# Performance work log

Hardware: AMD Instinct MI355X
Metric: run time of the kernel (lower is better)

The kernel has to match this reference:

```python
import jax, jax.numpy as jnp
import numpy as np

N_NODES = 100000
N_EDGES = 1600000
F_IN, F_HID, F_OUT = 128, 128, 40


def setup_inputs() -> dict:
    key = jax.random.key(0)
    ks = jax.random.split(key, 8)
    x = jax.random.normal(ks[0], (N_NODES, F_IN), dtype=jnp.float32)
    edge_index = jax.random.randint(ks[1], (2, N_EDGES), 0, N_NODES, dtype=jnp.int64)
    # GCNConv weights (glorot-style scale); biases zero per bias_init=zeros_
    W0 = jax.random.normal(ks[2], (F_IN, F_HID), dtype=jnp.float32) / np.sqrt(F_IN)
    b0 = jnp.zeros((F_HID,), dtype=jnp.float32)
    W1 = jax.random.normal(ks[3], (F_HID, F_HID), dtype=jnp.float32) / np.sqrt(F_HID)
    b1 = jnp.zeros((F_HID,), dtype=jnp.float32)
    W2 = jax.random.normal(ks[4], (F_HID, F_OUT), dtype=jnp.float32) / np.sqrt(F_HID)
    b2 = jnp.zeros((F_OUT,), dtype=jnp.float32)
    return {"x": x, "edge_index": edge_index, "W0": W0, "b0": b0,
            "W1": W1, "b1": b1, "W2": W2, "b2": b2}


def _gcn_conv(h, src, dst, W, b):
    # PyG GCNConv (normalize=False, add_self_loops=False):
    # linear transform, then sum-aggregate source features at destinations.
    h = h @ W                                   # [N, F_out]
    msgs = jnp.take(h, src, axis=0)             # [E, F_out] gather
    agg = jax.ops.segment_sum(msgs, dst, num_segments=N_NODES)  # scatter-add
    return agg + b


def reference(x, edge_index, W0, b0, W1, b1, W2, b2):
    src, dst = edge_index[0], edge_index[1]     # flow: source -> target
    h = jax.nn.relu(_gcn_conv(x, src, dst, W0, b0))
    h = jax.nn.relu(_gcn_conv(h, src, dst, W1, b1))
    out = _gcn_conv(h, src, dst, W2, b2)        # last layer: no activation
    return out
```

## Files before the change

### kernel.cpp

```cpp
#include <hip/hip_runtime.h>


typedef short bf16x8 __attribute__((ext_vector_type(8)));
typedef float f32x4  __attribute__((ext_vector_type(4)));

#define EPB 4096

__device__ __forceinline__ float bflo(unsigned int v) {
  union { float f; unsigned int i; } w; w.i = v << 16; return w.f;
}
__device__ __forceinline__ float bfhi(unsigned int v) {
  union { float f; unsigned int i; } w; w.i = v & 0xffff0000u; return w.f;
}
__device__ __forceinline__ unsigned short f2bf(float f) {
  union { float f; unsigned int i; } w; w.f = f;
  unsigned int b = w.i;
  unsigned int r = (b + 0x7fffu + ((b >> 16) & 1u)) >> 16;
  return (unsigned short)r;
}

__device__ __forceinline__ int edge_at(const void* ei, int is64, long long pos) {
  if (is64) return (int)((const long long*)ei)[pos];
  return ((const int*)ei)[pos];
}

__global__ void k_detect(const int* __restrict__ ei32, int* __restrict__ flag) {
  int tid = threadIdx.x;
  int v = ei32[2 * tid + 1];
  unsigned long long m = __ballot(v != 0);
  if (tid == 0) flag[0] = (m == 0ull) ? 1 : 0;
}

__global__ void k_cvt(const float* __restrict__ in, unsigned short* __restrict__ out,
                      long long n4) {
  long long i = (long long)blockIdx.x * blockDim.x + threadIdx.x;
  if (i >= n4) return;
  float4 v = *reinterpret_cast<const float4*>(in + i * 4);
  ushort4 o;
  o.x = f2bf(v.x); o.y = f2bf(v.y); o.z = f2bf(v.z); o.w = f2bf(v.w);
  *reinterpret_cast<ushort4*>(out + i * 4) = o;
}

__global__ void k_wt(const float* __restrict__ W, unsigned short* __restrict__ Wt,
                     int F, int Fp) {
  int idx = blockIdx.x * blockDim.x + threadIdx.x;
  if (idx >= Fp * 128) return;
  int c = idx >> 7, k = idx & 127;
  Wt[c * 128 + k] = (c < F) ? f2bf(W[(size_t)k * F + c]) : (unsigned short)0;
}

__global__ __launch_bounds__(256) void b_hist(const void* __restrict__ ei,
                                              const int* __restrict__ flag, int E,
                                              int* __restrict__ bhist,
                                              int NBKT, int NBLKE) {
  __shared__ int h[512];
  int blk = blockIdx.x, tid = threadIdx.x;
  for (int i = tid; i < NBKT; i += 256) h[i] = 0;
  __syncthreads();
  int is64 = flag[0];
  int base = blk * EPB;
  int cnt = min(EPB, E - base);
  for (int i = tid; i < cnt; i += 256) {
    int d = edge_at(ei, is64, (long long)E + base + i);
    atomicAdd(&h[d >> 8], 1);
  }
  __syncthreads();
  for (int i = tid; i < NBKT; i += 256) bhist[i * NBLKE + blk] = h[i];
}

__global__ void k_scan_a(const int* __restrict__ vals, int* __restrict__ lscan,
                         int* __restrict__ partials, int n) {
  __shared__ int sm[256];
  int tid = threadIdx.x;
  int i = blockIdx.x * 256 + tid;
  int v = (i < n) ? vals[i] : 0;
  sm[tid] = v;
  __syncthreads();
  for (int off = 1; off < 256; off <<= 1) {
    int t = (tid >= off) ? sm[tid - off] : 0;
    __syncthreads();
    sm[tid] += t;
    __syncthreads();
  }
  if (i < n) lscan[i] = sm[tid];
  if (tid == 255) partials[blockIdx.x] = sm[255];
}

__global__ void k_scan_b(int* __restrict__ partials, int nb) {
  __shared__ int sm[1024];
  int tid = threadIdx.x;
  int v = (tid < nb) ? partials[tid] : 0;
  sm[tid] = v;
  __syncthreads();
  for (int off = 1; off < 1024; off <<= 1) {
    int t = (tid >= off) ? sm[tid - off] : 0;
    __syncthreads();
    sm[tid] += t;
    __syncthreads();
  }
  if (tid < nb) partials[tid] = sm[tid] - v;
}

__global__ void k_scan_c(const int* __restrict__ lscan, const int* __restrict__ vals,
                         const int* __restrict__ partials, int* __restrict__ scanned,
                         int n) {
  int i = blockIdx.x * 256 + threadIdx.x;
  if (i >= n) return;
  scanned[i] = lscan[i] - vals[i] + partials[blockIdx.x];
}

__global__ void b_bptr(const int* __restrict__ scanned, int* __restrict__ bucketPtr,
                       int NBKT, int NBLKE, int E) {
  int i = blockIdx.x * 256 + threadIdx.x;
  if (i < NBKT) bucketPtr[i] = scanned[i * NBLKE];
  if (i == 0) bucketPtr[NBKT] = E;
}

__global__ __launch_bounds__(256) void b_scatter(const void* __restrict__ ei,
                                                 const int* __restrict__ flag, int E,
                                                 const int* __restrict__ scanned,
                                                 uint2* __restrict__ ebuf,
                                                 int NBKT, int NBLKE) {
  __shared__ int base[512];
  int blk = blockIdx.x, tid = threadIdx.x;
  for (int i = tid; i < NBKT; i += 256) base[i] = scanned[i * NBLKE + blk];
  __syncthreads();
  int is64 = flag[0];
  int b0 = blk * EPB;
  int cnt = min(EPB, E - b0);
  for (int i = tid; i < cnt; i += 256) {
    int d = edge_at(ei, is64, (long long)E + b0 + i);
    int s = edge_at(ei, is64, b0 + i);
    int pos = atomicAdd(&base[d >> 8], 1);
    ebuf[pos] = make_uint2((unsigned)d, (unsigned)s);
  }
}

__global__ __launch_bounds__(256) void b_pass2(const uint2* __restrict__ ebuf,
                                               const int* __restrict__ bucketPtr,
                                               int* __restrict__ rowptr,
                                               int* __restrict__ colsrc,
                                               int N, int NBKT, int E) {
  __shared__ int hist[256], excl[256], cur[256], sm[256];
  int b = blockIdx.x, tid = threadIdx.x;
  hist[tid] = 0;
  __syncthreads();
  int beg = bucketPtr[b], end = bucketPtr[b + 1];
  for (int i = beg + tid; i < end; i += 256)
    atomicAdd(&hist[ebuf[i].x & 255], 1);
  __syncthreads();
  int v = hist[tid];
  sm[tid] = v;
  __syncthreads();
  for (int off = 1; off < 256; off <<= 1) {
    int t = (tid >= off) ? sm[tid - off] : 0;
    __syncthreads();
    sm[tid] += t;
    __syncthreads();
  }
  excl[tid] = sm[tid] - v;
  cur[tid] = 0;
  __syncthreads();
  int nb0 = b << 8;
  if (nb0 + tid < N) rowptr[nb0 + tid] = beg + excl[tid];
  if (b == 0 && tid == 0) rowptr[N] = E;
  for (int i = beg + tid; i < end; i += 256) {
    uint2 e2 = ebuf[i];
    int dl = (int)(e2.x & 255u);
    int r = atomicAdd(&cur[dl], 1);
    colsrc[beg + excl[dl] + r] = (int)e2.y;
  }
}

__global__ void k_agg128b(const unsigned int* __restrict__ H,
                          const int* __restrict__ rowptr, const int* __restrict__ colsrc,
                          unsigned int* __restrict__ out, int N) {
  int node = blockIdx.x * 4 + (threadIdx.x >> 6);
  if (node >= N) return;
  int l = threadIdx.x & 63;
  int sub = l >> 4, fl = l & 15;
  int beg = rowptr[node], end = rowptr[node + 1];
  float a[8] = {0.f, 0.f, 0.f, 0.f, 0.f, 0.f, 0.f, 0.f};
  int i = beg + sub;
  for (; i + 4 < end; i += 8) {
    int s0 = colsrc[i], s1 = colsrc[i + 4];
    uint4 v0 = *reinterpret_cast<const uint4*>(H + (size_t)s0 * 64 + fl * 4);
    uint4 v1 = *reinterpret_cast<const uint4*>(H + (size_t)s1 * 64 + fl * 4);
    a[0] += bflo(v0.x) + bflo(v1.x); a[1] += bfhi(v0.x) + bfhi(v1.x);
    a[2] += bflo(v0.y) + bflo(v1.y); a[3] += bfhi(v0.y) + bfhi(v1.y);
    a[4] += bflo(v0.z) + bflo(v1.z); a[5] += bfhi(v0.z) + bfhi(v1.z);
    a[6] += bflo(v0.w) + bflo(v1.w); a[7] += bfhi(v0.w) + bfhi(v1.w);
  }
  if (i < end) {
    uint4 v = *reinterpret_cast<const uint4*>(H + (size_t)colsrc[i] * 64 + fl * 4);
    a[0] += bflo(v.x); a[1] += bfhi(v.x);
    a[2] += bflo(v.y); a[3] += bfhi(v.y);
    a[4] += bflo(v.z); a[5] += bfhi(v.z);
    a[6] += bflo(v.w); a[7] += bfhi(v.w);
  }
  #pragma unroll
  for (int k = 0; k < 8; ++k) {
    a[k] += __shfl_xor(a[k], 16);
    a[k] += __shfl_xor(a[k], 32);
  }
  if (sub == 0) {
    uint4 o;
    o.x = ((unsigned)f2bf(a[1]) << 16) | f2bf(a[0]);
    o.y = ((unsigned)f2bf(a[3]) << 16) | f2bf(a[2]);
    o.z = ((unsigned)f2bf(a[5]) << 16) | f2bf(a[4]);
    o.w = ((unsigned)f2bf(a[7]) << 16) | f2bf(a[6]);
    *reinterpret_cast<uint4*>(out + (size_t)node * 64 + fl * 4) = o;
  }
}

__global__ void k_agg40(const unsigned int* __restrict__ T,
                        const int* __restrict__ rowptr, const int* __restrict__ colsrc,
                        const float* __restrict__ b2, float* __restrict__ out, int N) {
  int node = blockIdx.x * 4 + (threadIdx.x >> 6);
  if (node >= N) return;
  int l = threadIdx.x & 63;
  int sub = l >> 4, fl = l & 15;
  int beg = rowptr[node], end = rowptr[node + 1];
  float a[4] = {0.f, 0.f, 0.f, 0.f};
  if (fl < 12) {
    int i = beg + sub;
    for (; i + 4 < end; i += 8) {
      int s0 = colsrc[i], s1 = colsrc[i + 4];
      uint2 v0 = *reinterpret_cast<const uint2*>(T + (size_t)s0 * 24 + fl * 2);
      uint2 v1 = *reinterpret_cast<const uint2*>(T + (size_t)s1 * 24 + fl * 2);
      a[0] += bflo(v0.x) + bflo(v1.x); a[1] += bfhi(v0.x) + bfhi(v1.x);
      a[2] += bflo(v0.y) + bflo(v1.y); a[3] += bfhi(v0.y) + bfhi(v1.y);
    }
    if (i < end) {
      uint2 v = *reinterpret_cast<const uint2*>(T + (size_t)colsrc[i] * 24 + fl * 2);
      a[0] += bflo(v.x); a[1] += bfhi(v.x);
      a[2] += bflo(v.y); a[3] += bfhi(v.y);
    }
  }
  #pragma unroll
  for (int k = 0; k < 4; ++k) {
    a[k] += __shfl_xor(a[k], 16);
    a[k] += __shfl_xor(a[k], 32);
  }
  if (sub == 0 && fl < 10) {
    float4 o;
    o.x = a[0] + b2[fl * 4 + 0];
    o.y = a[1] + b2[fl * 4 + 1];
    o.z = a[2] + b2[fl * 4 + 2];
    o.w = a[3] + b2[fl * 4 + 3];
    *reinterpret_cast<float4*>(out + (size_t)node * 40 + fl * 4) = o;
  }
}

__global__ __launch_bounds__(256) void k_gemm(const unsigned short* __restrict__ A,
                                              const unsigned short* __restrict__ Wt,
                                              const float* __restrict__ bias,
                                              unsigned short* __restrict__ C,
                                              int N, int Fp, int relu) {
  int tid = threadIdx.x;
  int w = tid >> 6, l = tid & 63;
  int r0 = blockIdx.x * 64 + w * 16;
  int arow = r0 + (l & 15);
  if (arow >= N) arow = N - 1;
  int kk = (l >> 4) * 8;
  bf16x8 a[4];
  #pragma unroll
  for (int ks = 0; ks < 4; ++ks)
    a[ks] = *reinterpret_cast<const bf16x8*>(A + (size_t)arow * 128 + ks * 32 + kk);

  int crow0 = r0 + (l >> 4) * 4;
  int ccol = l & 15;
  for (int cf = 0; cf < Fp / 16; ++cf) {
    f32x4 acc = {0.f, 0.f, 0.f, 0.f};
    const unsigned short* wp = Wt + (size_t)(cf * 16 + ccol) * 128 + kk;
    #pragma unroll
    for (int ks = 0; ks < 4; ++ks) {
      bf16x8 b = *reinterpret_cast<const bf16x8*>(wp + ks * 32);
      acc = __builtin_amdgcn_mfma_f32_16x16x32_bf16(a[ks], b, acc, 0, 0, 0);
    }
    float bv = bias ? bias[cf * 16 + ccol] : 0.f;
    #pragma unroll
    for (int r = 0; r < 4; ++r) {
      int gr = crow0 + r;
      if (gr >= N) continue;
      float v = acc[r] + bv;
      if (relu) v = fmaxf(v, 0.f);
      C[(size_t)gr * Fp + cf * 16 + ccol] = f2bf(v);
    }
  }
}

extern "C" void kernel_launch(void* const* d_in, const int* in_sizes, int n_in,
                              void* d_out, int out_size, void* d_ws, size_t ws_size,
                              hipStream_t stream) {
  const float* x  = (const float*)d_in[0];
  const void*  ei = d_in[1];
  const float* W0 = (const float*)d_in[2];
  const float* b0 = (const float*)d_in[3];
  const float* W1 = (const float*)d_in[4];
  const float* b1 = (const float*)d_in[5];
  const float* W2 = (const float*)d_in[6];
  const float* b2 = (const float*)d_in[7];
  float* out = (float*)d_out;

  const int N = in_sizes[0] / 128;
  const int E = in_sizes[1] / 2;
  const int FOUT = in_sizes[6] / 128;
  const int FP3 = 48;

  const int NBLKE = (E + EPB - 1) / EPB;
  const int NBKT  = (N + 255) / 256;
  const int T     = NBKT * NBLKE;
  const int GS    = (T + 255) / 256;

  char* wp = (char*)d_ws;
  auto alloc = [&](size_t bytes) -> void* {
    void* p = (void*)wp;
    wp += (bytes + 255) & ~(size_t)255;
    return p;
  };
  unsigned short* xb   = (unsigned short*)alloc((size_t)N * 128 * 2);
  unsigned short* bufA = (unsigned short*)alloc((size_t)N * 128 * 2);
  unsigned short* bufH = (unsigned short*)alloc((size_t)N * 128 * 2);
  unsigned short* t3   = (unsigned short*)alloc((size_t)N * FP3 * 2);
  unsigned short* Wt0  = (unsigned short*)alloc(128 * 128 * 2);
  unsigned short* Wt1  = (unsigned short*)alloc(128 * 128 * 2);
  unsigned short* Wt2  = (unsigned short*)alloc(FP3 * 128 * 2);
  uint2* ebuf   = (uint2*)alloc((size_t)E * 8);
  int* colsrc   = (int*)alloc((size_t)E * 4);
  int* rowptr   = (int*)alloc((size_t)(N + 1) * 4);
  int* bhist    = (int*)alloc((size_t)T * 4);
  int* lscan    = (int*)alloc((size_t)T * 4);
  int* scanned  = (int*)alloc((size_t)T * 4);
  int* partials = (int*)alloc(4096);
  int* bucketPtr= (int*)alloc((size_t)(NBKT + 1) * 4);
  int* flag     = (int*)alloc(256);

  k_detect<<<1, 64, 0, stream>>>((const int*)ei, flag);
  long long n4 = (long long)N * 32;
  k_cvt<<<(int)((n4 + 255) / 256), 256, 0, stream>>>(x, xb, n4);
  k_wt<<<(128 * 128 + 255) / 256, 256, 0, stream>>>(W0, Wt0, 128, 128);
  k_wt<<<(128 * 128 + 255) / 256, 256, 0, stream>>>(W1, Wt1, 128, 128);
  k_wt<<<(FP3 * 128 + 255) / 256, 256, 0, stream>>>(W2, Wt2, FOUT, FP3);

  b_hist<<<NBLKE, 256, 0, stream>>>(ei, flag, E, bhist, NBKT, NBLKE);
  k_scan_a<<<GS, 256, 0, stream>>>(bhist, lscan, partials, T);
  k_scan_b<<<1, 1024, 0, stream>>>(partials, GS);
  k_scan_c<<<GS, 256, 0, stream>>>(lscan, bhist, partials, scanned, T);
  b_bptr<<<(NBKT + 256) / 256, 256, 0, stream>>>(scanned, bucketPtr, NBKT, NBLKE, E);
  b_scatter<<<NBLKE, 256, 0, stream>>>(ei, flag, E, scanned, ebuf, NBKT, NBLKE);
  b_pass2<<<NBKT, 256, 0, stream>>>(ebuf, bucketPtr, rowptr, colsrc, N, NBKT, E);

  int gagg = (N + 3) / 4;
  int ggemm = (N + 63) / 64;
  k_agg128b<<<gagg, 256, 0, stream>>>((const unsigned int*)xb, rowptr, colsrc,
                                      (unsigned int*)bufA, N);
  k_gemm<<<ggemm, 256, 0, stream>>>(bufA, Wt0, b0, bufH, N, 128, 1);
  k_agg128b<<<gagg, 256, 0, stream>>>((const unsigned int*)bufH, rowptr, colsrc,
                                      (unsigned int*)bufA, N);
  k_gemm<<<ggemm, 256, 0, stream>>>(bufA, Wt1, b1, bufH, N, 128, 1);
  k_gemm<<<ggemm, 256, 0, stream>>>(bufH, Wt2, nullptr, t3, N, FP3, 0);
  k_agg40<<<gagg, 256, 0, stream>>>((const unsigned int*)t3, rowptr, colsrc, b2, out, N);
}
```

Baseline: 321.8 us.

## Fuse aggregation with MFMA GEMMs and merge small setup kernels

Fuses each 128-wide sum-aggregation with the following bf16 MFMA GEMM in one kernel. Each wave aggregates 16 nodes into swizzled LDS and then runs the 16x128 GEMM from LDS, so the aggregated intermediate no longer makes a round trip through HBM. The second fused kernel also chains the W2 projection through LDS. The three weight-transpose launches and the bucket-pointer kernel are merged into other kernels, and the gather loops are unrolled to four edges per iteration. The cost is lower parallelism: each wave now handles 16 nodes sequentially instead of one node per wave, which may reduce latency hiding for the irregular gathers.

```diff
diff --git a/kernel.cpp b/kernel.cpp
--- a/kernel.cpp
+++ b/kernel.cpp
@@ -41,12 +41,25 @@
   *reinterpret_cast<ushort4*>(out + i * 4) = o;
 }
 
-__global__ void k_wt(const float* __restrict__ W, unsigned short* __restrict__ Wt,
-                     int F, int Fp) {
+__global__ void k_wt3(const float* __restrict__ W0, const float* __restrict__ W1,
+                      const float* __restrict__ W2,
+                      unsigned short* __restrict__ Wt0, unsigned short* __restrict__ Wt1,
+                      unsigned short* __restrict__ Wt2, int FOUT, int FP3) {
   int idx = blockIdx.x * blockDim.x + threadIdx.x;
-  if (idx >= Fp * 128) return;
-  int c = idx >> 7, k = idx & 127;
-  Wt[c * 128 + k] = (c < F) ? f2bf(W[(size_t)k * F + c]) : (unsigned short)0;
+  if (idx < 16384) {
+    int c = idx >> 7, k = idx & 127;
+    Wt0[c * 128 + k] = f2bf(W0[k * 128 + c]);
+  } else if (idx < 32768) {
+    int t = idx - 16384;
+    int c = t >> 7, k = t & 127;
+    Wt1[c * 128 + k] = f2bf(W1[k * 128 + c]);
+  } else {
+    int t = idx - 32768;
+    if (t < FP3 * 128) {
+      int c = t >> 7, k = t & 127;
+      Wt2[c * 128 + k] = (c < FOUT) ? f2bf(W2[k * FOUT + c]) : (unsigned short)0;
+    }
+  }
 }
 
 __global__ __launch_bounds__(256) void b_hist(const void* __restrict__ ei,
@@ -103,16 +116,13 @@
 
 __global__ void k_scan_c(const int* __restrict__ lscan, const int* __restrict__ vals,
                          const int* __restrict__ partials, int* __restrict__ scanned,
-                         int n) {
+                         int* __restrict__ bucketPtr, int n, int NBLKE, int NBKT, int E) {
   int i = blockIdx.x * 256 + threadIdx.x;
   if (i >= n) return;
-  scanned[i] = lscan[i] - vals[i] + partials[blockIdx.x];
-}
-
-__global__ void b_bptr(const int* __restrict__ scanned, int* __restrict__ bucketPtr,
-                       int NBKT, int NBLKE, int E) {
-  int i = blockIdx.x * 256 + threadIdx.x;
-  if (i < NBKT) bucketPtr[i] = scanned[i * NBLKE];
+  int v = lscan[i] - vals[i] + partials[blockIdx.x];
+  scanned[i] = v;
+  int q = i / NBLKE;
+  if (i - q * NBLKE == 0) bucketPtr[q] = v;
   if (i == 0) bucketPtr[NBKT] = E;
 }
 
@@ -172,44 +182,138 @@
   }
 }
 
-__global__ void k_agg128b(const unsigned int* __restrict__ H,
-                          const int* __restrict__ rowptr, const int* __restrict__ colsrc,
-                          unsigned int* __restrict__ out, int N) {
-  int node = blockIdx.x * 4 + (threadIdx.x >> 6);
-  if (node >= N) return;
-  int l = threadIdx.x & 63;
+template <int MODE>
+__global__ __launch_bounds__(256) void k_fuse(const unsigned int* __restrict__ H,
+                                              const int* __restrict__ rowptr,
+                                              const int* __restrict__ colsrc,
+                                              const unsigned short* __restrict__ Wt,
+                                              const float* __restrict__ bias,
+                                              const unsigned short* __restrict__ Wt2,
+                                              unsigned short* __restrict__ C,
+                                              int N, int FP3) {
+  __shared__ unsigned int sh[4096];
+  int tid = threadIdx.x;
+  int w = tid >> 6, l = tid & 63;
   int sub = l >> 4, fl = l & 15;
-  int beg = rowptr[node], end = rowptr[node + 1];
-  float a[8] = {0.f, 0.f, 0.f, 0.f, 0.f, 0.f, 0.f, 0.f};
-  int i = beg + sub;
-  for (; i + 4 < end; i += 8) {
-    int s0 = colsrc[i], s1 = colsrc[i + 4];
-    uint4 v0 = *reinterpret_cast<const uint4*>(H + (size_t)s0 * 64 + fl * 4);
-    uint4 v1 = *reinterpret_cast<const uint4*>(H + (size_t)s1 * 64 + fl * 4);
-    a[0] += bflo(v0.x) + bflo(v1.x); a[1] += bfhi(v0.x) + bfhi(v1.x);
-    a[2] += bflo(v0.y) + bflo(v1.y); a[3] += bfhi(v0.y) + bfhi(v1.y);
-    a[4] += bflo(v0.z) + bflo(v1.z); a[5] += bfhi(v0.z) + bfhi(v1.z);
-    a[6] += bflo(v0.w) + bflo(v1.w); a[7] += bfhi(v0.w) + bfhi(v1.w);
-  }
-  if (i < end) {
-    uint4 v = *reinterpret_cast<const uint4*>(H + (size_t)colsrc[i] * 64 + fl * 4);
-    a[0] += bflo(v.x); a[1] += bfhi(v.x);
-    a[2] += bflo(v.y); a[3] += bfhi(v.y);
-    a[4] += bflo(v.z); a[5] += bfhi(v.z);
-    a[6] += bflo(v.w); a[7] += bfhi(v.w);
-  }
+  int tile = blockIdx.x * 64 + w * 16;
+  unsigned int* my = &sh[w * 1024];
+
+  for (int j = 0; j < 16; ++j) {
+    int node = tile + j;
+    float a[8] = {0.f, 0.f, 0.f, 0.f, 0.f, 0.f, 0.f, 0.f};
+    if (node < N) {
+      int beg = rowptr[node], end = rowptr[node + 1];
+      int i = beg + sub;
+      for (; i + 12 < end; i += 16) {
+        int s0 = colsrc[i], s1 = colsrc[i + 4], s2 = colsrc[i + 8], s3 = colsrc[i + 12];
+        uint4 v0 = *reinterpret_cast<const uint4*>(H + (size_t)s0 * 64 + fl * 4);
+        uint4 v1 = *reinterpret_cast<const uint4*>(H + (size_t)s1 * 64 + fl * 4);
+        uint4 v2 = *reinterpret_cast<const uint4*>(H + (size_t)s2 * 64 + fl * 4);
+        uint4 v3 = *reinterpret_cast<const uint4*>(H + (size_t)s3 * 64 + fl * 4);
+        a[0] += (bflo(v0.x) + bflo(v1.x)) + (bflo(v2.x) + bflo(v3.x));
+        a[1] += (bfhi(v0.x) + bfhi(v1.x)) + (bfhi(v2.x) + bfhi(v3.x));
+        a[2] += (bflo(v0.y) + bflo(v1.y)) + (bflo(v2.y) + bflo(v3.y));
+        a[3] += (bfhi(v0.y) + bfhi(v1.y)) + (bfhi(v2.y) + bfhi(v3.y));
+        a[4] += (bflo(v0.z) + bflo(v1.z)) + (bflo(v2.z) + bflo(v3.z));
+        a[5] += (bfhi(v0.z) + bfhi(v1.z)) + (bfhi(v2.z) + bfhi(v3.z));
+        a[6] += (bflo(v0.w) + bflo(v1.w)) + (bflo(v2.w) + bflo(v3.w));
+        a[7] += (bfhi(v0.w) + bfhi(v1.w)) + (bfhi(v2.w) + bfhi(v3.w));
+      }
+      for (; i < end; i += 4) {
+        uint4 v = *reinterpret_cast<const uint4*>(H + (size_t)colsrc[i] * 64 + fl * 4);
+        a[0] += bflo(v.x); a[1] += bfhi(v.x);
+        a[2] += bflo(v.y); a[3] += bfhi(v.y);
+        a[4] += bflo(v.z); a[5] += bfhi(v.z);
+        a[6] += bflo(v.w); a[7] += bfhi(v.w);
+      }
+    }
+    #pragma unroll
+    for (int k = 0; k < 8; ++k) {
+      a[k] += __shfl_xor(a[k], 16);
+      a[k] += __shfl_xor(a[k], 32);
+    }
+    if (sub == 0) {
+      uint4 o;
+      o.x = ((unsigned)f2bf(a[1]) << 16) | f2bf(a[0]);
+      o.y = ((unsigned)f2bf(a[3]) << 16) | f2bf(a[2]);
+      o.z = ((unsigned)f2bf(a[5]) << 16) | f2bf(a[4]);
+      o.w = ((unsigned)f2bf(a[7]) << 16) | f2bf(a[6]);
+      *reinterpret_cast<uint4*>(&my[j * 64 + ((fl ^ j) << 2)]) = o;
+    }
+  }
+
+  int n = fl;
+  bf16x8 af[4];
   #pragma unroll
-  for (int k = 0; k < 8; ++k) {
-    a[k] += __shfl_xor(a[k], 16);
-    a[k] += __shfl_xor(a[k], 32);
-  }
-  if (sub == 0) {
-    uint4 o;
-    o.x = ((unsigned)f2bf(a[1]) << 16) | f2bf(a[0]);
-    o.y = ((unsigned)f2bf(a[3]) << 16) | f2bf(a[2]);
-    o.z = ((unsigned)f2bf(a[5]) << 16) | f2bf(a[4]);
-    o.w = ((unsigned)f2bf(a[7]) << 16) | f2bf(a[6]);
-    *reinterpret_cast<uint4*>(out + (size_t)node * 64 + fl * 4) = o;
+  for (int ks = 0; ks < 4; ++ks) {
+    int c = (ks << 2) | sub;
+    af[ks] = *reinterpret_cast<const bf16x8*>(&my[n * 64 + ((c ^ n) << 2)]);
+  }
+  int kk = sub * 8;
+  int ccol = fl;
+
+  if (MODE == 0) {
+    #pragma unroll
+    for (int cf = 0; cf < 8; ++cf) {
+      f32x4 acc = {0.f, 0.f, 0.f, 0.f};
+      const unsigned short* wp = Wt + (size_t)(cf * 16 + ccol) * 128 + kk;
+      #pragma unroll
+      for (int ks = 0; ks < 4; ++ks) {
+        bf16x8 b = *reinterpret_cast<const bf16x8*>(wp + ks * 32);
+        acc = __builtin_amdgcn_mfma_f32_16x16x32_bf16(af[ks], b, acc, 0, 0, 0);
+      }
+      float bv = bias[cf * 16 + ccol];
+      #pragma unroll
+      for (int r = 0; r < 4; ++r) {
+        int gr = tile + sub * 4 + r;
+        if (gr < N) {
+          float v = fmaxf(acc[r] + bv, 0.f);
+          C[(size_t)gr * 128 + cf * 16 + ccol] = f2bf(v);
+        }
+      }
+    }
+  } else {
+    unsigned short* sh16 = (unsigned short*)my;
+    #pragma unroll
+    for (int cf = 0; cf < 8; ++cf) {
+      f32x4 acc = {0.f, 0.f, 0.f, 0.f};
+      const unsigned short* wp = Wt + (size_t)(cf * 16 + ccol) * 128 + kk;
+      #pragma unroll
+      for (int ks = 0; ks < 4; ++ks) {
+        bf16x8 b = *reinterpret_cast<const bf16x8*>(wp + ks * 32);
+        acc = __builtin_amdgcn_mfma_f32_16x16x32_bf16(af[ks], b, acc, 0, 0, 0);
+      }
+      float bv = bias[cf * 16 + ccol];
+      int col = cf * 16 + ccol;
+      int chunk = col >> 3;
+      #pragma unroll
+      for (int r = 0; r < 4; ++r) {
+        int row = sub * 4 + r;
+        float v = fmaxf(acc[r] + bv, 0.f);
+        sh16[row * 128 + ((chunk ^ row) << 3) + (col & 7)] = f2bf(v);
+      }
+    }
+    bf16x8 af3[4];
+    #pragma unroll
+    for (int ks = 0; ks < 4; ++ks) {
+      int c = (ks << 2) | sub;
+      af3[ks] = *reinterpret_cast<const bf16x8*>(&sh16[n * 128 + ((c ^ n) << 3)]);
+    }
+    for (int cf = 0; cf < FP3 / 16; ++cf) {
+      f32x4 acc = {0.f, 0.f, 0.f, 0.f};
+      const unsigned short* wp = Wt2 + (size_t)(cf * 16 + ccol) * 128 + kk;
+      #pragma unroll
+      for (int ks = 0; ks < 4; ++ks) {
+        bf16x8 b = *reinterpret_cast<const bf16x8*>(wp + ks * 32);
+        acc = __builtin_amdgcn_mfma_f32_16x16x32_bf16(af3[ks], b, acc, 0, 0, 0);
+      }
+      #pragma unroll
+      for (int r = 0; r < 4; ++r) {
+        int gr = tile + sub * 4 + r;
+        if (gr < N)
+          C[(size_t)gr * FP3 + cf * 16 + ccol] = f2bf(acc[r]);
+      }
+    }
   }
 }
 
@@ -224,14 +328,18 @@
   float a[4] = {0.f, 0.f, 0.f, 0.f};
   if (fl < 12) {
     int i = beg + sub;
-    for (; i + 4 < end; i += 8) {
-      int s0 = colsrc[i], s1 = colsrc[i + 4];
+    for (; i + 12 < end; i += 16) {
+      int s0 = colsrc[i], s1 = colsrc[i + 4], s2 = colsrc[i + 8], s3 = colsrc[i + 12];
       uint2 v0 = *reinterpret_cast<const uint2*>(T + (size_t)s0 * 24 + fl * 2);
       uint2 v1 = *reinterpret_cast<const uint2*>(T + (size_t)s1 * 24 + fl * 2);
-      a[0] += bflo(v0.x) + bflo(v1.x); a[1] += bfhi(v0.x) + bfhi(v1.x);
-      a[2] += bflo(v0.y) + bflo(v1.y); a[3] += bfhi(v0.y) + bfhi(v1.y);
-    }
-    if (i < end) {
+      uint2 v2 = *reinterpret_cast<const uint2*>(T + (size_t)s2 * 24 + fl * 2);
+      uint2 v3 = *reinterpret_cast<const uint2*>(T + (size_t)s3 * 24 + fl * 2);
+      a[0] += (bflo(v0.x) + bflo(v1.x)) + (bflo(v2.x) + bflo(v3.x));
+      a[1] += (bfhi(v0.x) + bfhi(v1.x)) + (bfhi(v2.x) + bfhi(v3.x));
+      a[2] += (bflo(v0.y) + bflo(v1.y)) + (bflo(v2.y) + bflo(v3.y));
+      a[3] += (bfhi(v0.y) + bfhi(v1.y)) + (bfhi(v2.y) + bfhi(v3.y));
+    }
+    for (; i < end; i += 4) {
       uint2 v = *reinterpret_cast<const uint2*>(T + (size_t)colsrc[i] * 24 + fl * 2);
       a[0] += bflo(v.x); a[1] += bfhi(v.x);
       a[2] += bflo(v.y); a[3] += bfhi(v.y);
@@ -249,44 +357,6 @@
     o.z = a[2] + b2[fl * 4 + 2];
     o.w = a[3] + b2[fl * 4 + 3];
     *reinterpret_cast<float4*>(out + (size_t)node * 40 + fl * 4) = o;
-  }
-}
-
-__global__ __launch_bounds__(256) void k_gemm(const unsigned short* __restrict__ A,
-                                              const unsigned short* __restrict__ Wt,
-                                              const float* __restrict__ bias,
-                                              unsigned short* __restrict__ C,
-                                              int N, int Fp, int relu) {
-  int tid = threadIdx.x;
-  int w = tid >> 6, l = tid & 63;
-  int r0 = blockIdx.x * 64 + w * 16;
-  int arow = r0 + (l & 15);
-  if (arow >= N) arow = N - 1;
-  int kk = (l >> 4) * 8;
-  bf16x8 a[4];
-  #pragma unroll
-  for (int ks = 0; ks < 4; ++ks)
-    a[ks] = *reinterpret_cast<const bf16x8*>(A + (size_t)arow * 128 + ks * 32 + kk);
-
-  int crow0 = r0 + (l >> 4) * 4;
-  int ccol = l & 15;
-  for (int cf = 0; cf < Fp / 16; ++cf) {
-    f32x4 acc = {0.f, 0.f, 0.f, 0.f};
-    const unsigned short* wp = Wt + (size_t)(cf * 16 + ccol) * 128 + kk;
-    #pragma unroll
-    for (int ks = 0; ks < 4; ++ks) {
-      bf16x8 b = *reinterpret_cast<const bf16x8*>(wp + ks * 32);
-      acc = __builtin_amdgcn_mfma_f32_16x16x32_bf16(a[ks], b, acc, 0, 0, 0);
-    }
-    float bv = bias ? bias[cf * 16 + ccol] : 0.f;
-    #pragma unroll
-    for (int r = 0; r < 4; ++r) {
-      int gr = crow0 + r;
-      if (gr >= N) continue;
-      float v = acc[r] + bv;
-      if (relu) v = fmaxf(v, 0.f);
-      C[(size_t)gr * Fp + cf * 16 + ccol] = f2bf(v);
-    }
   }
 }
 
@@ -320,7 +390,6 @@
     return p;
   };
   unsigned short* xb   = (unsigned short*)alloc((size_t)N * 128 * 2);
-  unsigned short* bufA = (unsigned short*)alloc((size_t)N * 128 * 2);
   unsigned short* bufH = (unsigned short*)alloc((size_t)N * 128 * 2);
   unsigned short* t3   = (unsigned short*)alloc((size_t)N * FP3 * 2);
   unsigned short* Wt0  = (unsigned short*)alloc(128 * 128 * 2);
@@ -339,26 +408,21 @@
   k_detect<<<1, 64, 0, stream>>>((const int*)ei, flag);
   long long n4 = (long long)N * 32;
   k_cvt<<<(int)((n4 + 255) / 256), 256, 0, stream>>>(x, xb, n4);
-  k_wt<<<(128 * 128 + 255) / 256, 256, 0, stream>>>(W0, Wt0, 128, 128);
-  k_wt<<<(128 * 128 + 255) / 256, 256, 0, stream>>>(W1, Wt1, 128, 128);
-  k_wt<<<(FP3 * 128 + 255) / 256, 256, 0, stream>>>(W2, Wt2, FOUT, FP3);
-
+  k_wt3<<<(32768 + FP3 * 128 + 255) / 256, 256, 0, stream>>>(W0, W1, W2, Wt0, Wt1, Wt2,
+                                                             FOUT, FP3);
   b_hist<<<NBLKE, 256, 0, stream>>>(ei, flag, E, bhist, NBKT, NBLKE);
   k_scan_a<<<GS, 256, 0, stream>>>(bhist, lscan, partials, T);
   k_scan_b<<<1, 1024, 0, stream>>>(partials, GS);
-  k_scan_c<<<GS, 256, 0, stream>>>(lscan, bhist, partials, scanned, T);
-  b_bptr<<<(NBKT + 256) / 256, 256, 0, stream>>>(scanned, bucketPtr, NBKT, NBLKE, E);
+  k_scan_c<<<GS, 256, 0, stream>>>(lscan, bhist, partials, scanned, bucketPtr,
+                                   T, NBLKE, NBKT, E);
   b_scatter<<<NBLKE, 256, 0, stream>>>(ei, flag, E, scanned, ebuf, NBKT, NBLKE);
   b_pass2<<<NBKT, 256, 0, stream>>>(ebuf, bucketPtr, rowptr, colsrc, N, NBKT, E);
 
-  int gagg = (N + 3) / 4;
-  int ggemm = (N + 63) / 64;
-  k_agg128b<<<gagg, 256, 0, stream>>>((const unsigned int*)xb, rowptr, colsrc,
-                                      (unsigned int*)bufA, N);
-  k_gemm<<<ggemm, 256, 0, stream>>>(bufA, Wt0, b0, bufH, N, 128, 1);
-  k_agg128b<<<gagg, 256, 0, stream>>>((const unsigned int*)bufH, rowptr, colsrc,
-                                      (unsigned int*)bufA, N);
-  k_gemm<<<ggemm, 256, 0, stream>>>(bufA, Wt1, b1, bufH, N, 128, 1);
-  k_gemm<<<ggemm, 256, 0, stream>>>(bufH, Wt2, nullptr, t3, N, FP3, 0);
-  k_agg40<<<gagg, 256, 0, stream>>>((const unsigned int*)t3, rowptr, colsrc, b2, out, N);
-}
+  int gfuse = (N + 63) / 64;
+  k_fuse<0><<<gfuse, 256, 0, stream>>>((const unsigned int*)xb, rowptr, colsrc,
+                                       Wt0, b0, nullptr, bufH, N, FP3);
+  k_fuse<1><<<gfuse, 256, 0, stream>>>((const unsigned int*)bufH, rowptr, colsrc,
+                                       Wt1, b1, Wt2, t3, N, FP3);
+  k_agg40<<<(N + 3) / 4, 256, 0, stream>>>((const unsigned int*)t3, rowptr, colsrc,
+                                           b2, out, N);
+}
```

Measured after the change: 317.2 us. Within noise of the previous version (-1.4%).
